# Performance work log

Measured on AMD Instinct MI355X. Metric: run time of the kernel, lower is better.

## Reference

```python
import jax, jax.numpy as jnp
import numpy as np

DIM = 768
H = 12
HD = DIM // H  # 64
B = 16
N = 1025  # cls token + 1024 patches; RoPE applied to tokens 1:


def setup_inputs() -> dict:
    key = jax.random.key(0)
    k1, k2, k3, k4, k5, k6 = jax.random.split(key, 6)
    x = jax.random.normal(k1, (B, N, DIM), dtype=jnp.float32)
    # rotary angles for the N-1 non-cls tokens, HD//2 freq pairs
    theta = jax.random.uniform(k2, (N - 1, HD // 2), dtype=jnp.float32) * 2.0 * jnp.pi
    freqs_cos = jnp.cos(theta)
    freqs_sin = jnp.sin(theta)
    W_qkv = jax.random.normal(k3, (3 * DIM, DIM), dtype=jnp.float32) * 0.02
    W_proj = jax.random.normal(k4, (DIM, DIM), dtype=jnp.float32) * 0.02
    b_proj = jax.random.normal(k5, (DIM,), dtype=jnp.float32) * 0.02
    return {"x": x, "freqs_cos": freqs_cos, "freqs_sin": freqs_sin,
            "W_qkv": W_qkv, "W_proj": W_proj, "b_proj": b_proj}


def _apply_rope(t, cos, sin):
    # t: [b, h, m, d]; cos/sin: [m, d/2]. Pairs are interleaved (even, odd),
    # matching torch.view_as_complex on a (..., d/2, 2) reshape.
    tr = t[..., 0::2]
    ti = t[..., 1::2]
    cos = cos[None, None, :, :]
    sin = sin[None, None, :, :]
    out_r = tr * cos - ti * sin
    out_i = tr * sin + ti * cos
    # interleave back: (..., d/2, 2) -> (..., d)
    out = jnp.stack([out_r, out_i], axis=-1)
    return out.reshape(t.shape)


def reference(x, freqs_cos, freqs_sin, W_qkv, W_proj, b_proj):
    b, n, dim = x.shape
    h, hd = H, HD
    scale = hd ** -0.5

    qkv = jnp.einsum('bnd,ed->bne', x, W_qkv)            # [b, n, 3*dim]
    qkv = qkv.reshape(b, n, 3, h, hd)
    q = jnp.transpose(qkv[:, :, 0], (0, 2, 1, 3))         # [b, h, n, hd]
    k = jnp.transpose(qkv[:, :, 1], (0, 2, 1, 3))
    v = jnp.transpose(qkv[:, :, 2], (0, 2, 1, 3))

    # RoPE on all tokens except the cls token (index 0)
    q = jnp.concatenate([q[:, :, :1], _apply_rope(q[:, :, 1:], freqs_cos, freqs_sin)], axis=2)
    k = jnp.concatenate([k[:, :, :1], _apply_rope(k[:, :, 1:], freqs_cos, freqs_sin)], axis=2)

    dots = jnp.einsum('bhid,bhjd->bhij', q, k) * scale    # [b, h, n, n]
    attn = jax.nn.softmax(dots, axis=-1)
    out = jnp.einsum('bhij,bhjd->bhid', attn, v)          # [b, h, n, hd]
    out = jnp.transpose(out, (0, 2, 1, 3)).reshape(b, n, dim)
    out = jnp.einsum('bnd,ed->bne', out, W_proj) + b_proj
    return out
```

## Files before the change

kernel.cpp:

```cpp
#include <hip/hip_runtime.h>
#include <stdint.h>

#define NH 12
#define HD64 64
#define SEQ 1025
#define M_ROWS (16 * SEQ)
#define DIM 768
#define NPAD 1088

typedef __attribute__((ext_vector_type(8))) short bf16x8;
typedef __attribute__((ext_vector_type(4))) float f32x4;
typedef __attribute__((ext_vector_type(4))) short s16x4;

__device__ __forceinline__ short f2bf_rne(float f) {
    union { float f; uint32_t u; } c; c.f = f;
    uint32_t u = c.u + 0x7fffu + ((c.u >> 16) & 1u);
    return (short)(u >> 16);
}

__device__ __forceinline__ int cvt_pk_bf16(float lo, float hi) {
    int r;
    asm("v_cvt_pk_bf16_f32 %0, %1, %2" : "=v"(r) : "v"(lo), "v"(hi));
    return r;
}

__device__ __forceinline__ void gload_lds16(const void* g, void* l) {
    __builtin_amdgcn_global_load_lds(
        (const __attribute__((address_space(1))) void*)g,
        (__attribute__((address_space(3))) void*)l, 16, 0, 0);
}

__global__ void f2bf_kernel(const float* __restrict__ in, short* __restrict__ out, int n4) {
    int i = blockIdx.x * blockDim.x + threadIdx.x;
    if (i < n4) {
        f32x4 f = ((const f32x4*)in)[i];
        s16x4 o;
        o[0] = f2bf_rne(f[0]); o[1] = f2bf_rne(f[1]);
        o[2] = f2bf_rne(f[2]); o[3] = f2bf_rne(f[3]);
        ((s16x4*)out)[i] = o;
    }
}

__global__ __launch_bounds__(256) void qkv_gemm_kernel(
    const short* __restrict__ xb, const short* __restrict__ wb,
    const float* __restrict__ fcos, const float* __restrict__ fsin,
    short* __restrict__ Qb, short* __restrict__ Kb, short* __restrict__ VTb)
{
    __shared__ short Alds[128 * 32];
    __shared__ short Blds[128 * 32];
    const int tid = threadIdx.x;
    const int lane = tid & 63, w = tid >> 6;
    const int wm = w >> 1, wn = w & 1;
    const int lr = lane & 15, lg = lane >> 4;
    const int mt = blockIdx.x, nt = blockIdx.y;

    f32x4 acc[4][4];
#pragma unroll
    for (int i = 0; i < 4; i++)
#pragma unroll
        for (int j = 0; j < 4; j++) acc[i][j] = (f32x4)0.0f;

    for (int kt = 0; kt < 24; ++kt) {
        __syncthreads();
#pragma unroll
        for (int i = 0; i < 2; i++) {
            int c = i * 256 + tid;
            int row = c >> 2, cc = c & 3;
            int gr = mt * 128 + row; if (gr > M_ROWS - 1) gr = M_ROWS - 1;
            gload_lds16(xb + (size_t)gr * DIM + kt * 32 + cc * 8, Alds + c * 8);
            int gb = nt * 128 + row;
            gload_lds16(wb + (size_t)gb * DIM + kt * 32 + cc * 8, Blds + c * 8);
        }
        asm volatile("s_waitcnt vmcnt(0)" ::: "memory");
        __syncthreads();

        bf16x8 af[4], bfr[4];
#pragma unroll
        for (int mi = 0; mi < 4; mi++)
            af[mi] = *(const bf16x8*)&Alds[(wm * 64 + mi * 16 + lr) * 32 + lg * 8];
#pragma unroll
        for (int ni = 0; ni < 4; ni++)
            bfr[ni] = *(const bf16x8*)&Blds[(wn * 64 + ni * 16 + lr) * 32 + lg * 8];
#pragma unroll
        for (int mi = 0; mi < 4; mi++)
#pragma unroll
            for (int ni = 0; ni < 4; ni++)
                acc[mi][ni] = __builtin_amdgcn_mfma_f32_16x16x32_bf16(af[mi], bfr[ni], acc[mi][ni], 0, 0, 0);
    }

#pragma unroll
    for (int ni = 0; ni < 4; ni++) {
        int e = nt * 128 + wn * 64 + ni * 16 + lr;
        int qkv = e / DIM;
        int rem = e - qkv * DIM;
        int h = rem >> 6, d = rem & 63;
#pragma unroll
        for (int mi = 0; mi < 4; mi++) {
            f32x4 v4 = acc[mi][ni];
#pragma unroll
            for (int j = 0; j < 4; j++) {
                int m = mt * 128 + wm * 64 + mi * 16 + lg * 4 + j;
                float v = v4[j];
                float vo = __shfl_xor(v, 1);
                bool valid = (m < M_ROWS);
                int mm = valid ? m : 0;
                int b = mm / SEQ;
                int n = mm - b * SEQ;
                float outv = v;
                if (qkv < 2 && n > 0) {
                    float cs = fcos[(n - 1) * 32 + (d >> 1)];
                    float sn = fsin[(n - 1) * 32 + (d >> 1)];
                    outv = (d & 1) ? (vo * sn + v * cs) : (v * cs - vo * sn);
                }
                if (qkv == 0) outv *= 0.180336881f;
                if (valid) {
                    short bv = f2bf_rne(outv);
                    size_t bh = (size_t)b * NH + h;
                    if (qkv == 0)      Qb[(bh * SEQ + n) * HD64 + d] = bv;
                    else if (qkv == 1) Kb[(bh * SEQ + n) * HD64 + d] = bv;
                    else               VTb[(bh * HD64 + d) * NPAD + n] = bv;
                }
            }
        }
    }
}

__global__ __launch_bounds__(256) void attn_kernel(
    const short* __restrict__ Qb, const short* __restrict__ Kb,
    const short* __restrict__ VTb, short* __restrict__ AO)
{
    __shared__ short Klds[64 * 64];
    __shared__ short Vlds[64 * 64];
    __shared__ int Plds[4][16 * 32];
    const int tid = threadIdx.x;
    const int lane = tid & 63, w = tid >> 6;
    const int lr = lane & 15, lg = lane >> 4;
    const int qt = blockIdx.x, bh = blockIdx.y;
    const int b = bh / NH, h = bh - b * NH;

    const short* Qp = Qb + (size_t)bh * SEQ * HD64;
    const short* Kp = Kb + (size_t)bh * SEQ * HD64;
    const short* Vp = VTb + (size_t)bh * HD64 * NPAD;

    int qr = qt * 64 + w * 16 + lr; if (qr > SEQ - 1) qr = SEQ - 1;
    bf16x8 qf0 = *(const bf16x8*)&Qp[(size_t)qr * HD64 + 0 + lg * 8];
    bf16x8 qf1 = *(const bf16x8*)&Qp[(size_t)qr * HD64 + 32 + lg * 8];

    float m_i = -1e30f, l_i = 0.f;
    f32x4 acc[4];
#pragma unroll
    for (int vt = 0; vt < 4; vt++) acc[vt] = (f32x4)0.0f;

    int* pw = &Plds[w][0];
    const int pswz = (lr & 3) << 3;

    for (int t = 0; t < 17; ++t) {
        __syncthreads();
        int k0 = t * 64;
#pragma unroll
        for (int i = 0; i < 2; i++) {
            int c = i * 256 + tid;
            int row = c >> 3, ccd = c & 7;
            int cl = ccd ^ (row & 7);
            int krow = k0 + row; if (krow > SEQ - 1) krow = SEQ - 1;
            gload_lds16(Kp + (size_t)krow * HD64 + cl * 8, Klds + c * 8);
            gload_lds16(Vp + (size_t)row * NPAD + k0 + cl * 8, Vlds + c * 8);
        }
        asm volatile("s_waitcnt vmcnt(0)" ::: "memory");
        __syncthreads();

        f32x4 s[4];
#pragma unroll
        for (int k16 = 0; k16 < 4; k16++) {
            int krow = k16 * 16 + lr;
            bf16x8 kf0 = *(const bf16x8*)&Klds[krow * 64 + ((0 + lg) ^ (krow & 7)) * 8];
            bf16x8 kf1 = *(const bf16x8*)&Klds[krow * 64 + ((4 + lg) ^ (krow & 7)) * 8];
            f32x4 d = (f32x4)0.0f;
            d = __builtin_amdgcn_mfma_f32_16x16x32_bf16(kf0, qf0, d, 0, 0, 0);
            d = __builtin_amdgcn_mfma_f32_16x16x32_bf16(kf1, qf1, d, 0, 0, 0);
            s[k16] = d;
        }
        if (t == 16) {
            s[0][0] = (lg == 0) ? s[0][0] : -1e30f;
            s[0][1] = -1e30f; s[0][2] = -1e30f; s[0][3] = -1e30f;
#pragma unroll
            for (int k16 = 1; k16 < 4; k16++) { s[k16][0] = -1e30f; s[k16][1] = -1e30f; s[k16][2] = -1e30f; s[k16][3] = -1e30f; }
        }

        float a0 = fmaxf(s[0][0], s[0][1]), a1 = fmaxf(s[0][2], s[0][3]);
        float a2 = fmaxf(s[1][0], s[1][1]), a3 = fmaxf(s[1][2], s[1][3]);
        float a4 = fmaxf(s[2][0], s[2][1]), a5 = fmaxf(s[2][2], s[2][3]);
        float a6 = fmaxf(s[3][0], s[3][1]), a7 = fmaxf(s[3][2], s[3][3]);
        float b0 = fmaxf(fmaxf(a0, a1), fmaxf(a2, a3));
        float b1 = fmaxf(fmaxf(a4, a5), fmaxf(a6, a7));
        float pmax = fmaxf(b0, b1);
        pmax = fmaxf(pmax, __shfl_xor(pmax, 16));
        pmax = fmaxf(pmax, __shfl_xor(pmax, 32));

        if (__any(pmax > m_i + 11.54f)) {
            float mnew = fmaxf(m_i, pmax);
            float sc = exp2f(m_i - mnew);
            m_i = mnew;
            l_i *= sc;
#pragma unroll
            for (int j = 0; j < 4; j++) {
                float scj = __shfl(sc, 4 * lg + j);
#pragma unroll
                for (int vt = 0; vt < 4; vt++) acc[vt][j] *= scj;
            }
        }

#pragma unroll
        for (int k16 = 0; k16 < 4; k16++) {
#pragma unroll
            for (int j = 0; j < 4; j++) s[k16][j] = exp2f(s[k16][j] - m_i);
        }
        float r0 = (s[0][0] + s[0][1]) + (s[0][2] + s[0][3]);
        float r1 = (s[1][0] + s[1][1]) + (s[1][2] + s[1][3]);
        float r2 = (s[2][0] + s[2][1]) + (s[2][2] + s[2][3]);
        float r3 = (s[3][0] + s[3][1]) + (s[3][2] + s[3][3]);
        float rowsum = (r0 + r1) + (r2 + r3);
        rowsum += __shfl_xor(rowsum, 16);
        rowsum += __shfl_xor(rowsum, 32);
        l_i += rowsum;

#pragma unroll
        for (int k16 = 0; k16 < 4; k16++) {
            int pk0 = cvt_pk_bf16(s[k16][0], s[k16][1]);
            int pk1 = cvt_pk_bf16(s[k16][2], s[k16][3]);
            int pbase = 8 * k16 + 2 * lg;
            pw[lr * 32 + ((pbase + 0) ^ pswz)] = pk0;
            pw[lr * 32 + ((pbase + 1) ^ pswz)] = pk1;
        }
        bf16x8 pa0 = *(const bf16x8*)&pw[lr * 32 + ((4 * lg) ^ pswz)];
        bf16x8 pa1 = *(const bf16x8*)&pw[lr * 32 + ((16 + 4 * lg) ^ pswz)];

#pragma unroll
        for (int vt = 0; vt < 4; vt++) {
            int dr = vt * 16 + lr;
            bf16x8 vf0 = *(const bf16x8*)&Vlds[dr * 64 + ((0 + lg) ^ (dr & 7)) * 8];
            bf16x8 vf1 = *(const bf16x8*)&Vlds[dr * 64 + ((4 + lg) ^ (dr & 7)) * 8];
            acc[vt] = __builtin_amdgcn_mfma_f32_16x16x32_bf16(pa0, vf0, acc[vt], 0, 0, 0);
            acc[vt] = __builtin_amdgcn_mfma_f32_16x16x32_bf16(pa1, vf1, acc[vt], 0, 0, 0);
        }
    }

    float inv[4];
#pragma unroll
    for (int j = 0; j < 4; j++) inv[j] = 1.0f / __shfl(l_i, 4 * lg + j);
#pragma unroll
    for (int vt = 0; vt < 4; vt++) {
#pragma unroll
        for (int j = 0; j < 4; j++) {
            int qrow = qt * 64 + w * 16 + lg * 4 + j;
            if (qrow < SEQ) {
                AO[((size_t)(b * SEQ + qrow)) * DIM + h * HD64 + vt * 16 + lr] =
                    f2bf_rne(acc[vt][j] * inv[j]);
            }
        }
    }
}

__global__ __launch_bounds__(256) void proj_gemm_kernel(
    const short* __restrict__ ab, const short* __restrict__ wb,
    const float* __restrict__ bias, float* __restrict__ out)
{
    __shared__ short Alds[128 * 32];
    __shared__ short Blds[128 * 32];
    const int tid = threadIdx.x;
    const int lane = tid & 63, w = tid >> 6;
    const int wm = w >> 1, wn = w & 1;
    const int lr = lane & 15, lg = lane >> 4;
    const int mt = blockIdx.x, nt = blockIdx.y;

    f32x4 acc[4][4];
#pragma unroll
    for (int i = 0; i < 4; i++)
#pragma unroll
        for (int j = 0; j < 4; j++) acc[i][j] = (f32x4)0.0f;

    for (int kt = 0; kt < 24; ++kt) {
        __syncthreads();
#pragma unroll
        for (int i = 0; i < 2; i++) {
            int c = i * 256 + tid;
            int row = c >> 2, cc = c & 3;
            int gr = mt * 128 + row; if (gr > M_ROWS - 1) gr = M_ROWS - 1;
            gload_lds16(ab + (size_t)gr * DIM + kt * 32 + cc * 8, Alds + c * 8);
            int gb = nt * 128 + row;
            gload_lds16(wb + (size_t)gb * DIM + kt * 32 + cc * 8, Blds + c * 8);
        }
        asm volatile("s_waitcnt vmcnt(0)" ::: "memory");
        __syncthreads();

        bf16x8 af[4], bfr[4];
#pragma unroll
        for (int mi = 0; mi < 4; mi++)
            af[mi] = *(const bf16x8*)&Alds[(wm * 64 + mi * 16 + lr) * 32 + lg * 8];
#pragma unroll
        for (int ni = 0; ni < 4; ni++)
            bfr[ni] = *(const bf16x8*)&Blds[(wn * 64 + ni * 16 + lr) * 32 + lg * 8];
#pragma unroll
        for (int mi = 0; mi < 4; mi++)
#pragma unroll
            for (int ni = 0; ni < 4; ni++)
                acc[mi][ni] = __builtin_amdgcn_mfma_f32_16x16x32_bf16(af[mi], bfr[ni], acc[mi][ni], 0, 0, 0);
    }

#pragma unroll
    for (int ni = 0; ni < 4; ni++) {
        int e = nt * 128 + wn * 64 + ni * 16 + lr;
        float bv = bias[e];
#pragma unroll
        for (int mi = 0; mi < 4; mi++) {
#pragma unroll
            for (int j = 0; j < 4; j++) {
                int m = mt * 128 + wm * 64 + mi * 16 + lg * 4 + j;
                if (m < M_ROWS) out[(size_t)m * DIM + e] = acc[mi][ni][j] + bv;
            }
        }
    }
}

extern "C" void kernel_launch(void* const* d_in, const int* in_sizes, int n_in,
                              void* d_out, int out_size, void* d_ws, size_t ws_size,
                              hipStream_t stream) {
    const float* x     = (const float*)d_in[0];
    const float* fcos  = (const float*)d_in[1];
    const float* fsin  = (const float*)d_in[2];
    const float* wqkv  = (const float*)d_in[3];
    const float* wproj = (const float*)d_in[4];
    const float* bproj = (const float*)d_in[5];
    float* out = (float*)d_out;

    char* ws = (char*)d_ws;
    size_t off = 0;
    auto salloc = [&](size_t bytes) { void* p = ws + off; off += (bytes + 255) & ~(size_t)255; return p; };
    short* xb     = (short*)salloc((size_t)M_ROWS * DIM * 2);
    short* wqkvb  = (short*)salloc((size_t)2304 * DIM * 2);
    short* wprojb = (short*)salloc((size_t)DIM * DIM * 2);
    short* Qb     = (short*)salloc((size_t)192 * SEQ * HD64 * 2);
    short* Kb     = (short*)salloc((size_t)192 * SEQ * HD64 * 2);
    short* VTb    = (short*)salloc((size_t)192 * HD64 * NPAD * 2);
    short* AO     = (short*)salloc((size_t)M_ROWS * DIM * 2);

    {
        int n4 = M_ROWS * DIM / 4;
        f2bf_kernel<<<(n4 + 255) / 256, 256, 0, stream>>>(x, xb, n4);
    }
    {
        int n4 = 2304 * DIM / 4;
        f2bf_kernel<<<(n4 + 255) / 256, 256, 0, stream>>>(wqkv, wqkvb, n4);
    }
    {
        int n4 = DIM * DIM / 4;
        f2bf_kernel<<<(n4 + 255) / 256, 256, 0, stream>>>(wproj, wprojb, n4);
    }

    qkv_gemm_kernel<<<dim3(129, 18), 256, 0, stream>>>(xb, wqkvb, fcos, fsin, Qb, Kb, VTb);
    attn_kernel<<<dim3(17, 192), 256, 0, stream>>>(Qb, Kb, VTb, AO);
    proj_gemm_kernel<<<dim3(129, 6), 256, 0, stream>>>(AO, wprojb, bproj, out);
}
```

Before: 382.2 us.

## Double-buffer LDS tiles and remap workgroups per XCD in all three kernels

Converts the QKV GEMM, attention, and projection GEMM main loops to double-buffered LDS, so the next tile's global-to-LDS load is issued before computing on the current one. This hides load latency behind MFMA work and drops one barrier per iteration. Launches become 1D grids with a chunked XCD swizzle, so neighbouring tiles that share operands land on the same XCD and its L2. Doubling LDS per block may reduce occupancy, and the QKV epilogue loop order is also swapped to hoist the row index math.

```diff
diff --git a/kernel.cpp b/kernel.cpp
--- a/kernel.cpp
+++ b/kernel.cpp
@@ -28,6 +28,13 @@
     __builtin_amdgcn_global_load_lds(
         (const __attribute__((address_space(1))) void*)g,
         (__attribute__((address_space(3))) void*)l, 16, 0, 0);
+}
+
+__device__ __forceinline__ int xcd_chunk_swizzle(int orig, int nwg) {
+    int q = nwg >> 3, r = nwg & 7;
+    int xcd = orig & 7, i = orig >> 3;
+    int start = (xcd < r) ? xcd * (q + 1) : r * (q + 1) + (xcd - r) * q;
+    return start + i;
 }
 
 __global__ void f2bf_kernel(const float* __restrict__ in, short* __restrict__ out, int n4) {
@@ -46,13 +53,14 @@
     const float* __restrict__ fcos, const float* __restrict__ fsin,
     short* __restrict__ Qb, short* __restrict__ Kb, short* __restrict__ VTb)
 {
-    __shared__ short Alds[128 * 32];
-    __shared__ short Blds[128 * 32];
+    __shared__ short Alds[2][128 * 32];
+    __shared__ short Blds[2][128 * 32];
     const int tid = threadIdx.x;
     const int lane = tid & 63, w = tid >> 6;
     const int wm = w >> 1, wn = w & 1;
     const int lr = lane & 15, lg = lane >> 4;
-    const int mt = blockIdx.x, nt = blockIdx.y;
+    const int tile = xcd_chunk_swizzle(blockIdx.x, 129 * 18);
+    const int mt = tile / 18, nt = tile - (tile / 18) * 18;
 
     f32x4 acc[4][4];
 #pragma unroll
@@ -60,52 +68,61 @@
 #pragma unroll
         for (int j = 0; j < 4; j++) acc[i][j] = (f32x4)0.0f;
 
-    for (int kt = 0; kt < 24; ++kt) {
-        __syncthreads();
+    auto stage = [&](int buf, int kt) {
 #pragma unroll
         for (int i = 0; i < 2; i++) {
             int c = i * 256 + tid;
             int row = c >> 2, cc = c & 3;
             int gr = mt * 128 + row; if (gr > M_ROWS - 1) gr = M_ROWS - 1;
-            gload_lds16(xb + (size_t)gr * DIM + kt * 32 + cc * 8, Alds + c * 8);
+            gload_lds16(xb + (size_t)gr * DIM + kt * 32 + cc * 8, &Alds[buf][c * 8]);
             int gb = nt * 128 + row;
-            gload_lds16(wb + (size_t)gb * DIM + kt * 32 + cc * 8, Blds + c * 8);
-        }
+            gload_lds16(wb + (size_t)gb * DIM + kt * 32 + cc * 8, &Blds[buf][c * 8]);
+        }
+    };
+
+    stage(0, 0);
+    asm volatile("s_waitcnt vmcnt(0)" ::: "memory");
+    __syncthreads();
+
+    for (int kt = 0; kt < 24; ++kt) {
+        int cur = kt & 1;
+        if (kt < 23) stage(cur ^ 1, kt + 1);
+
+        bf16x8 af[4], bfr[4];
+#pragma unroll
+        for (int mi = 0; mi < 4; mi++)
+            af[mi] = *(const bf16x8*)&Alds[cur][(wm * 64 + mi * 16 + lr) * 32 + lg * 8];
+#pragma unroll
+        for (int ni = 0; ni < 4; ni++)
+            bfr[ni] = *(const bf16x8*)&Blds[cur][(wn * 64 + ni * 16 + lr) * 32 + lg * 8];
+#pragma unroll
+        for (int mi = 0; mi < 4; mi++)
+#pragma unroll
+            for (int ni = 0; ni < 4; ni++)
+                acc[mi][ni] = __builtin_amdgcn_mfma_f32_16x16x32_bf16(af[mi], bfr[ni], acc[mi][ni], 0, 0, 0);
+
         asm volatile("s_waitcnt vmcnt(0)" ::: "memory");
         __syncthreads();
-
-        bf16x8 af[4], bfr[4];
-#pragma unroll
-        for (int mi = 0; mi < 4; mi++)
-            af[mi] = *(const bf16x8*)&Alds[(wm * 64 + mi * 16 + lr) * 32 + lg * 8];
-#pragma unroll
-        for (int ni = 0; ni < 4; ni++)
-            bfr[ni] = *(const bf16x8*)&Blds[(wn * 64 + ni * 16 + lr) * 32 + lg * 8];
-#pragma unroll
-        for (int mi = 0; mi < 4; mi++)
-#pragma unroll
-            for (int ni = 0; ni < 4; ni++)
-                acc[mi][ni] = __builtin_amdgcn_mfma_f32_16x16x32_bf16(af[mi], bfr[ni], acc[mi][ni], 0, 0, 0);
-    }
-
-#pragma unroll
-    for (int ni = 0; ni < 4; ni++) {
-        int e = nt * 128 + wn * 64 + ni * 16 + lr;
-        int qkv = e / DIM;
-        int rem = e - qkv * DIM;
-        int h = rem >> 6, d = rem & 63;
-#pragma unroll
-        for (int mi = 0; mi < 4; mi++) {
-            f32x4 v4 = acc[mi][ni];
-#pragma unroll
-            for (int j = 0; j < 4; j++) {
-                int m = mt * 128 + wm * 64 + mi * 16 + lg * 4 + j;
-                float v = v4[j];
+    }
+
+#pragma unroll
+    for (int mi = 0; mi < 4; mi++) {
+        int mbase = mt * 128 + wm * 64 + mi * 16 + lg * 4;
+#pragma unroll
+        for (int j = 0; j < 4; j++) {
+            int m = mbase + j;
+            bool valid = (m < M_ROWS);
+            int mm = valid ? m : 0;
+            int b = mm / SEQ;
+            int n = mm - b * SEQ;
+#pragma unroll
+            for (int ni = 0; ni < 4; ni++) {
+                int e = nt * 128 + wn * 64 + ni * 16 + lr;
+                int qkv = e / DIM;
+                int rem = e - qkv * DIM;
+                int h = rem >> 6, d = rem & 63;
+                float v = acc[mi][ni][j];
                 float vo = __shfl_xor(v, 1);
-                bool valid = (m < M_ROWS);
-                int mm = valid ? m : 0;
-                int b = mm / SEQ;
-                int n = mm - b * SEQ;
                 float outv = v;
                 if (qkv < 2 && n > 0) {
                     float cs = fcos[(n - 1) * 32 + (d >> 1)];
@@ -129,13 +146,14 @@
     const short* __restrict__ Qb, const short* __restrict__ Kb,
     const short* __restrict__ VTb, short* __restrict__ AO)
 {
-    __shared__ short Klds[64 * 64];
-    __shared__ short Vlds[64 * 64];
+    __shared__ short Klds[2][64 * 64];
+    __shared__ short Vlds[2][64 * 64];
     __shared__ int Plds[4][16 * 32];
     const int tid = threadIdx.x;
     const int lane = tid & 63, w = tid >> 6;
     const int lr = lane & 15, lg = lane >> 4;
-    const int qt = blockIdx.x, bh = blockIdx.y;
+    const int tile = xcd_chunk_swizzle(blockIdx.x, 17 * 192);
+    const int bh = tile / 17, qt = tile - (tile / 17) * 17;
     const int b = bh / NH, h = bh - b * NH;
 
     const short* Qp = Qb + (size_t)bh * SEQ * HD64;
@@ -154,8 +172,7 @@
     int* pw = &Plds[w][0];
     const int pswz = (lr & 3) << 3;
 
-    for (int t = 0; t < 17; ++t) {
-        __syncthreads();
+    auto stageKV = [&](int buf, int t) {
         int k0 = t * 64;
 #pragma unroll
         for (int i = 0; i < 2; i++) {
@@ -163,18 +180,25 @@
             int row = c >> 3, ccd = c & 7;
             int cl = ccd ^ (row & 7);
             int krow = k0 + row; if (krow > SEQ - 1) krow = SEQ - 1;
-            gload_lds16(Kp + (size_t)krow * HD64 + cl * 8, Klds + c * 8);
-            gload_lds16(Vp + (size_t)row * NPAD + k0 + cl * 8, Vlds + c * 8);
-        }
-        asm volatile("s_waitcnt vmcnt(0)" ::: "memory");
-        __syncthreads();
+            gload_lds16(Kp + (size_t)krow * HD64 + cl * 8, &Klds[buf][c * 8]);
+            gload_lds16(Vp + (size_t)row * NPAD + k0 + cl * 8, &Vlds[buf][c * 8]);
+        }
+    };
+
+    stageKV(0, 0);
+    asm volatile("s_waitcnt vmcnt(0)" ::: "memory");
+    __syncthreads();
+
+    for (int t = 0; t < 17; ++t) {
+        int cur = t & 1;
+        if (t < 16) stageKV(cur ^ 1, t + 1);
 
         f32x4 s[4];
 #pragma unroll
         for (int k16 = 0; k16 < 4; k16++) {
             int krow = k16 * 16 + lr;
-            bf16x8 kf0 = *(const bf16x8*)&Klds[krow * 64 + ((0 + lg) ^ (krow & 7)) * 8];
-            bf16x8 kf1 = *(const bf16x8*)&Klds[krow * 64 + ((4 + lg) ^ (krow & 7)) * 8];
+            bf16x8 kf0 = *(const bf16x8*)&Klds[cur][krow * 64 + ((0 + lg) ^ (krow & 7)) * 8];
+            bf16x8 kf1 = *(const bf16x8*)&Klds[cur][krow * 64 + ((4 + lg) ^ (krow & 7)) * 8];
             f32x4 d = (f32x4)0.0f;
             d = __builtin_amdgcn_mfma_f32_16x16x32_bf16(kf0, qf0, d, 0, 0, 0);
             d = __builtin_amdgcn_mfma_f32_16x16x32_bf16(kf1, qf1, d, 0, 0, 0);
@@ -238,11 +262,14 @@
 #pragma unroll
         for (int vt = 0; vt < 4; vt++) {
             int dr = vt * 16 + lr;
-            bf16x8 vf0 = *(const bf16x8*)&Vlds[dr * 64 + ((0 + lg) ^ (dr & 7)) * 8];
-            bf16x8 vf1 = *(const bf16x8*)&Vlds[dr * 64 + ((4 + lg) ^ (dr & 7)) * 8];
+            bf16x8 vf0 = *(const bf16x8*)&Vlds[cur][dr * 64 + ((0 + lg) ^ (dr & 7)) * 8];
+            bf16x8 vf1 = *(const bf16x8*)&Vlds[cur][dr * 64 + ((4 + lg) ^ (dr & 7)) * 8];
             acc[vt] = __builtin_amdgcn_mfma_f32_16x16x32_bf16(pa0, vf0, acc[vt], 0, 0, 0);
             acc[vt] = __builtin_amdgcn_mfma_f32_16x16x32_bf16(pa1, vf1, acc[vt], 0, 0, 0);
         }
+
+        asm volatile("s_waitcnt vmcnt(0)" ::: "memory");
+        __syncthreads();
     }
 
     float inv[4];
@@ -265,13 +292,14 @@
     const short* __restrict__ ab, const short* __restrict__ wb,
     const float* __restrict__ bias, float* __restrict__ out)
 {
-    __shared__ short Alds[128 * 32];
-    __shared__ short Blds[128 * 32];
+    __shared__ short Alds[2][128 * 32];
+    __shared__ short Blds[2][128 * 32];
     const int tid = threadIdx.x;
     const int lane = tid & 63, w = tid >> 6;
     const int wm = w >> 1, wn = w & 1;
     const int lr = lane & 15, lg = lane >> 4;
-    const int mt = blockIdx.x, nt = blockIdx.y;
+    const int tile = xcd_chunk_swizzle(blockIdx.x, 129 * 6);
+    const int mt = tile / 6, nt = tile - (tile / 6) * 6;
 
     f32x4 acc[4][4];
 #pragma unroll
@@ -279,32 +307,41 @@
 #pragma unroll
         for (int j = 0; j < 4; j++) acc[i][j] = (f32x4)0.0f;
 
-    for (int kt = 0; kt < 24; ++kt) {
-        __syncthreads();
+    auto stage = [&](int buf, int kt) {
 #pragma unroll
         for (int i = 0; i < 2; i++) {
             int c = i * 256 + tid;
             int row = c >> 2, cc = c & 3;
             int gr = mt * 128 + row; if (gr > M_ROWS - 1) gr = M_ROWS - 1;
-            gload_lds16(ab + (size_t)gr * DIM + kt * 32 + cc * 8, Alds + c * 8);
+            gload_lds16(ab + (size_t)gr * DIM + kt * 32 + cc * 8, &Alds[buf][c * 8]);
             int gb = nt * 128 + row;
-            gload_lds16(wb + (size_t)gb * DIM + kt * 32 + cc * 8, Blds + c * 8);
-        }
+            gload_lds16(wb + (size_t)gb * DIM + kt * 32 + cc * 8, &Blds[buf][c * 8]);
+        }
+    };
+
+    stage(0, 0);
+    asm volatile("s_waitcnt vmcnt(0)" ::: "memory");
+    __syncthreads();
+
+    for (int kt = 0; kt < 24; ++kt) {
+        int cur = kt & 1;
+        if (kt < 23) stage(cur ^ 1, kt + 1);
+
+        bf16x8 af[4], bfr[4];
+#pragma unroll
+        for (int mi = 0; mi < 4; mi++)
+            af[mi] = *(const bf16x8*)&Alds[cur][(wm * 64 + mi * 16 + lr) * 32 + lg * 8];
+#pragma unroll
+        for (int ni = 0; ni < 4; ni++)
+            bfr[ni] = *(const bf16x8*)&Blds[cur][(wn * 64 + ni * 16 + lr) * 32 + lg * 8];
+#pragma unroll
+        for (int mi = 0; mi < 4; mi++)
+#pragma unroll
+            for (int ni = 0; ni < 4; ni++)
+                acc[mi][ni] = __builtin_amdgcn_mfma_f32_16x16x32_bf16(af[mi], bfr[ni], acc[mi][ni], 0, 0, 0);
+
         asm volatile("s_waitcnt vmcnt(0)" ::: "memory");
         __syncthreads();
-
-        bf16x8 af[4], bfr[4];
-#pragma unroll
-        for (int mi = 0; mi < 4; mi++)
-            af[mi] = *(const bf16x8*)&Alds[(wm * 64 + mi * 16 + lr) * 32 + lg * 8];
-#pragma unroll
-        for (int ni = 0; ni < 4; ni++)
-            bfr[ni] = *(const bf16x8*)&Blds[(wn * 64 + ni * 16 + lr) * 32 + lg * 8];
-#pragma unroll
-        for (int mi = 0; mi < 4; mi++)
-#pragma unroll
-            for (int ni = 0; ni < 4; ni++)
-                acc[mi][ni] = __builtin_amdgcn_mfma_f32_16x16x32_bf16(af[mi], bfr[ni], acc[mi][ni], 0, 0, 0);
     }
 
 #pragma unroll
@@ -357,7 +394,7 @@
         f2bf_kernel<<<(n4 + 255) / 256, 256, 0, stream>>>(wproj, wprojb, n4);
     }
 
-    qkv_gemm_kernel<<<dim3(129, 18), 256, 0, stream>>>(xb, wqkvb, fcos, fsin, Qb, Kb, VTb);
-    attn_kernel<<<dim3(17, 192), 256, 0, stream>>>(Qb, Kb, VTb, AO);
-    proj_gemm_kernel<<<dim3(129, 6), 256, 0, stream>>>(AO, wprojb, bproj, out);
-}
+    qkv_gemm_kernel<<<129 * 18, 256, 0, stream>>>(xb, wqkvb, fcos, fsin, Qb, Kb, VTb);
+    attn_kernel<<<17 * 192, 256, 0, stream>>>(Qb, Kb, VTb, AO);
+    proj_gemm_kernel<<<129 * 6, 256, 0, stream>>>(AO, wprojb, bproj, out);
+}
```

New measurement: 355.8 us. 1.07x faster.
